# Kernel tuning notes

Hardware: AMD Instinct MI355X
Metric: run time of the kernel (lower is better)

The kernel has to match this reference:

```python
import jax, jax.numpy as jnp
import numpy as np

N_NODES = 100000
NEG_SLOPE = 0.2


def _gat_conv(x, edge_index, W, att_src, att_dst, bias):
    """Single-head PyG-style GATConv with self-loops.
    x: [N, F_in], edge_index: [2, E] (row 0 = src j, row 1 = dst i).
    """
    N = x.shape[0]
    h = x @ W  # [N, F_out]
    # add self-loops
    loop = jnp.arange(N, dtype=edge_index.dtype)
    src = jnp.concatenate([edge_index[0], loop])
    dst = jnp.concatenate([edge_index[1], loop])
    # per-node attention terms, gathered per edge
    a_s = h @ att_src  # [N]
    a_d = h @ att_dst  # [N]
    e = jax.nn.leaky_relu(a_s[src] + a_d[dst], NEG_SLOPE)  # [E+N]
    # segment softmax over incoming edges of each destination
    m = jax.ops.segment_max(e, dst, num_segments=N)  # [N]
    m = jnp.where(jnp.isfinite(m), m, 0.0)
    p = jnp.exp(e - m[dst])
    denom = jax.ops.segment_sum(p, dst, num_segments=N)  # [N], >0 due to self-loops
    alpha = p / denom[dst]  # [E+N]
    # scatter-aggregate weighted source features
    out = jax.ops.segment_sum(h[src] * alpha[:, None], dst, num_segments=N)
    return out + bias


def setup_inputs() -> dict:
    key = jax.random.key(0)
    ks = jax.random.split(key, 12)
    F_in, H, C = 128, 64, 40
    x = jax.random.normal(ks[0], (N_NODES, F_in), dtype=jnp.float32)
    edge_index = jax.random.randint(ks[1], (2, 1600000), 0, N_NODES, dtype=jnp.int64)
    s1 = 1.0 / np.sqrt(F_in)
    s2 = 1.0 / np.sqrt(H)
    return {
        "x": x,
        "edge_index": edge_index,
        "W1": jax.random.uniform(ks[2], (F_in, H), jnp.float32, -s1, s1),
        "att_src1": jax.random.uniform(ks[3], (H,), jnp.float32, -s2, s2),
        "att_dst1": jax.random.uniform(ks[4], (H,), jnp.float32, -s2, s2),
        "b1": jnp.zeros((H,), jnp.float32),
        "W2": jax.random.uniform(ks[5], (H, C), jnp.float32, -s2, s2),
        "att_src2": jax.random.uniform(ks[6], (C,), jnp.float32, -1.0 / np.sqrt(C), 1.0 / np.sqrt(C)),
        "att_dst2": jax.random.uniform(ks[7], (C,), jnp.float32, -1.0 / np.sqrt(C), 1.0 / np.sqrt(C)),
        "b2": jnp.zeros((C,), jnp.float32),
    }


def reference(x, edge_index, W1, att_src1, att_dst1, b1, W2, att_src2, att_dst2, b2):
    h = _gat_conv(x, edge_index, W1, att_src1, att_dst1, b1)
    h = jax.nn.relu(h)
    # dropout is identity in eval mode
    out = _gat_conv(h, edge_index, W2, att_src2, att_dst2, b2)
    return out
```

## Files before the change

kernel.cpp:

```cpp
#include <hip/hip_runtime.h>
#include <math.h>


#define NEG_SLOPE 0.2f
#define BIN_SHIFT 8
#define BIN_NODES 256
#define MAXBINS   512
#define CAPB      4864
#define K1_CHUNK  4096
#define MAXDEG    128
#define AGG_STRIDE 132
#define XS1 136

typedef _Float16 h4_t __attribute__((ext_vector_type(4)));
typedef _Float16 h8_t __attribute__((ext_vector_type(8)));
typedef float    f16x_t __attribute__((ext_vector_type(16)));

__device__ __forceinline__ float lrelu(float v) {
    return v > 0.f ? v : NEG_SLOPE * v;
}

__global__ __launch_bounds__(256) void prep_kernel(
    const float* __restrict__ W1, const float* __restrict__ W2,
    const float* __restrict__ as1, const float* __restrict__ ad1,
    const float* __restrict__ as2, const float* __restrict__ ad2,
    _Float16* __restrict__ w1t, _Float16* __restrict__ w2t,
    float* __restrict__ u1, float* __restrict__ v1,
    int* __restrict__ bin_cursor)
{
    const int tid = threadIdx.x;
    if (blockIdx.x == 0) {
        for (int j = tid; j < MAXBINS; j += 256) bin_cursor[j] = 0;
        for (int i = tid; i < 8192; i += 256) {
            int n = i >> 7, k = i & 127;
            w1t[i] = (_Float16)W1[k * 64 + n];
        }
        if (tid < 128) {
            float su = 0.f, sv = 0.f;
            for (int n = 0; n < 64; ++n) {
                float w = W1[tid * 64 + n];
                su += w * as1[n];
                sv += w * ad1[n];
            }
            u1[tid] = su; v1[tid] = sv;
        }
    } else {
        __shared__ float u2l[64], v2l[64];
        if (tid < 64) {
            float su = 0.f, sv = 0.f;
            for (int n = 0; n < 40; ++n) {
                float w = W2[tid * 40 + n];
                su += w * as2[n];
                sv += w * ad2[n];
            }
            u2l[tid] = su; v2l[tid] = sv;
        }
        __syncthreads();
        for (int i = tid; i < 4096; i += 256) {
            int n = i >> 6, k = i & 63;
            _Float16 o = (_Float16)0.f;
            if (n < 40)       o = (_Float16)W2[k * 40 + n];
            else if (n == 40) o = (_Float16)u2l[k];
            else if (n == 41) o = (_Float16)v2l[k];
            w2t[i] = o;
        }
    }
}

__global__ __launch_bounds__(256) void gemm1_bin_kernel(
    const float* __restrict__ x, const _Float16* __restrict__ w1t,
    const float* __restrict__ u1, const float* __restrict__ v1,
    _Float16* __restrict__ h, float* __restrict__ as_, float* __restrict__ ad_,
    int N, int gb,
    const int* __restrict__ src, const int* __restrict__ dst, int E, int nbins,
    int* __restrict__ bin_cursor, int* __restrict__ binned)
{
    __shared__ __align__(16) char smem[35840];
    const int tid = threadIdx.x;

    if (blockIdx.x < gb) {
        _Float16* Xs = (_Float16*)smem;
        _Float16* Wt = (_Float16*)(smem + 17408);
        float*    Us = (float*)(smem + 34816);
        float*    Vs = (float*)(smem + 35328);
        const int lane = tid & 63;
        const int w = tid >> 6;
        const int rh = w >> 1, ch = w & 1;
        const long rowbase = (long)blockIdx.x * 64;

        {
            const int4* s4 = (const int4*)w1t;
#pragma unroll
            for (int i = 0; i < 4; ++i) {
                int f = tid + i * 256;
                int n = f >> 4, c = f & 15;
                *(int4*)&Wt[n * XS1 + c * 8] = s4[f];
            }
        }
        {
            const float4* X4 = (const float4*)x;
            const long gmax = (long)N * 32;
#pragma unroll
            for (int i = 0; i < 8; ++i) {
                int f = tid + i * 256;
                int row = f >> 5, c4 = f & 31;
                long gi = (rowbase + row) * 32 + c4;
                float4 v = (gi < gmax) ? X4[gi] : make_float4(0.f, 0.f, 0.f, 0.f);
                h4_t hv;
                hv.x = (_Float16)v.x; hv.y = (_Float16)v.y;
                hv.z = (_Float16)v.z; hv.w = (_Float16)v.w;
                *(h4_t*)&Xs[row * XS1 + c4 * 4] = hv;
            }
        }
        if (tid < 128) Us[tid] = u1[tid];
        else { int t = tid - 128; Vs[t] = v1[t]; }
        __syncthreads();

        {
            const int arow = tid >> 2, apart = tid & 3;
            const _Float16* xr = &Xs[arow * XS1 + apart * 32];
            float ps = 0.f, pd = 0.f;
#pragma unroll
            for (int k = 0; k < 32; k += 4) {
                h4_t xv = *(const h4_t*)(xr + k);
                float4 uu = *(const float4*)&Us[apart * 32 + k];
                float4 vv = *(const float4*)&Vs[apart * 32 + k];
                float x0 = (float)xv.x, x1 = (float)xv.y, x2 = (float)xv.z, x3 = (float)xv.w;
                ps += x0 * uu.x + x1 * uu.y + x2 * uu.z + x3 * uu.w;
                pd += x0 * vv.x + x1 * vv.y + x2 * vv.z + x3 * vv.w;
            }
            ps += __shfl_xor(ps, 1); ps += __shfl_xor(ps, 2);
            pd += __shfl_xor(pd, 1); pd += __shfl_xor(pd, 2);
            if (apart == 0 && rowbase + arow < N) {
                as_[rowbase + arow] = ps;
                ad_[rowbase + arow] = pd;
            }
        }

        const int m = lane & 31, khalf = lane >> 5;
        const _Float16* ax = &Xs[(rh * 32 + m) * XS1 + khalf * 8];
        const _Float16* bx = &Wt[(ch * 32 + m) * XS1 + khalf * 8];

        f16x_t acc = {};
#pragma unroll
        for (int kc = 0; kc < 8; ++kc) {
            h8_t a = *(const h8_t*)(ax + kc * 16);
            h8_t b = *(const h8_t*)(bx + kc * 16);
            acc = __builtin_amdgcn_mfma_f32_32x32x16_f16(a, b, acc, 0, 0, 0);
        }

        const int col = ch * 32 + m;
#pragma unroll
        for (int r = 0; r < 16; ++r) {
            int rowl = (r & 3) + 8 * (r >> 2) + 4 * khalf;
            long grow = rowbase + rh * 32 + rowl;
            if (grow < N) h[grow * 64 + col] = (_Float16)acc[r];
        }
    } else {
        int* hist = (int*)smem;
        int* base = (int*)(smem + 2048);
        int* lcur = (int*)(smem + 4096);
        const int e0 = (blockIdx.x - gb) * K1_CHUNK;

        int sreg[16], dreg[16];
#pragma unroll
        for (int k = 0; k < 16; ++k) {
            int e = e0 + tid + k * 256;
            bool ok = e < E;
            dreg[k] = ok ? dst[e] : -1;
            sreg[k] = ok ? src[e] : 0;
        }

        for (int j = tid; j < nbins; j += 256) hist[j] = 0;
        __syncthreads();
#pragma unroll
        for (int k = 0; k < 16; ++k)
            if (dreg[k] >= 0) atomicAdd(&hist[dreg[k] >> BIN_SHIFT], 1);
        __syncthreads();
        for (int j = tid; j < nbins; j += 256) {
            int c = hist[j];
            base[j] = (c > 0) ? atomicAdd(&bin_cursor[j], c) : 0;
            lcur[j] = 0;
        }
        __syncthreads();
#pragma unroll
        for (int k = 0; k < 16; ++k) {
            if (dreg[k] >= 0) {
                int b = dreg[k] >> BIN_SHIFT;
                int o = atomicAdd(&lcur[b], 1);
                int pos = base[b] + o;
                if (pos < CAPB)
                    binned[b * CAPB + pos] =
                        (sreg[k] << BIN_SHIFT) | (dreg[k] & (BIN_NODES - 1));
            }
        }
    }
}

__global__ __launch_bounds__(512) void fine_kernel(
    const int* __restrict__ bin_cursor, const int* __restrict__ binned,
    int* __restrict__ csr, int* __restrict__ rowptr, int N, int nbins)
{
    __shared__ int a[MAXBINS];
    __shared__ int nh[BIN_NODES];
    __shared__ int cur[BIN_NODES];
    __shared__ int sb[2];
    const int b = blockIdx.x;
    const int tid = threadIdx.x;

    int v = (tid < nbins) ? min(bin_cursor[tid], CAPB) : 0;
    a[tid] = v;
    __syncthreads();
#pragma unroll
    for (int ofs = 1; ofs < MAXBINS; ofs <<= 1) {
        int t = (tid >= ofs) ? a[tid - ofs] : 0;
        __syncthreads();
        a[tid] += t;
        __syncthreads();
    }
    if (tid == 0) {
        sb[0] = (b > 0) ? a[b - 1] : 0;
        sb[1] = a[nbins - 1];
    }

    const int cnt = min(bin_cursor[b], CAPB);
    const int nn = min(BIN_NODES, N - b * BIN_NODES);
    const int* __restrict__ brec = binned + (long)b * CAPB;

    if (tid < BIN_NODES) nh[tid] = 0;
    __syncthreads();

    for (int k = tid; k < cnt; k += 512) {
        atomicAdd(&nh[brec[k] & (BIN_NODES - 1)], 1);
    }
    __syncthreads();

    int hv = (tid < BIN_NODES) ? nh[tid] : 0;
#pragma unroll
    for (int ofs = 1; ofs < BIN_NODES; ofs <<= 1) {
        int t = (tid >= ofs && tid < BIN_NODES) ? nh[tid - ofs] : 0;
        __syncthreads();
        if (tid < BIN_NODES) nh[tid] += t;
        __syncthreads();
    }
    const int binbase = sb[0];
    if (tid < BIN_NODES) {
        int excl = nh[tid] - hv;
        if (tid < nn) rowptr[b * BIN_NODES + tid] = binbase + excl;
        cur[tid] = binbase + excl;
    }
    if (b == nbins - 1 && tid == 0) rowptr[N] = sb[1];
    __syncthreads();

    for (int k = tid; k < cnt; k += 512) {
        int rec = brec[k];
        int pos = atomicAdd(&cur[rec & (BIN_NODES - 1)], 1);
        csr[pos] = rec >> BIN_SHIFT;
    }
}

#define XS2 72
__global__ __launch_bounds__(256) void gemm2_kernel(
    const _Float16* __restrict__ hin, const _Float16* __restrict__ w2t,
    _Float16* __restrict__ h2, float* __restrict__ as_, float* __restrict__ ad_,
    int N)
{
    __shared__ __align__(16) _Float16 Xs[64 * XS2];
    __shared__ __align__(16) _Float16 Wt[64 * XS2];
    const int tid = threadIdx.x;
    const int lane = tid & 63;
    const int w = tid >> 6;
    const int rh = w >> 1, ch = w & 1;
    const long rowbase = (long)blockIdx.x * 64;

    {
        const int4* s4 = (const int4*)w2t;
#pragma unroll
        for (int i = 0; i < 2; ++i) {
            int f = tid + i * 256;
            int n = f >> 3, c = f & 7;
            *(int4*)&Wt[n * XS2 + c * 8] = s4[f];
        }
    }
    {
        const h8_t* X8 = (const h8_t*)hin;
        const long gmax = (long)N * 8;
#pragma unroll
        for (int i = 0; i < 2; ++i) {
            int f = tid + i * 256;
            int row = f >> 3, c = f & 7;
            long gi = (rowbase + row) * 8 + c;
            h8_t v = {};
            if (gi < gmax) v = X8[gi];
#pragma unroll
            for (int j = 0; j < 8; ++j) v[j] = (v[j] > (_Float16)0.f) ? v[j] : (_Float16)0.f;
            *(h8_t*)&Xs[row * XS2 + c * 8] = v;
        }
    }
    __syncthreads();

    const int m = lane & 31, khalf = lane >> 5;
    const _Float16* ax = &Xs[(rh * 32 + m) * XS2 + khalf * 8];
    const _Float16* bx = &Wt[(ch * 32 + m) * XS2 + khalf * 8];

    f16x_t acc = {};
#pragma unroll
    for (int kc = 0; kc < 4; ++kc) {
        h8_t a = *(const h8_t*)(ax + kc * 16);
        h8_t b = *(const h8_t*)(bx + kc * 16);
        acc = __builtin_amdgcn_mfma_f32_32x32x16_f16(a, b, acc, 0, 0, 0);
    }

    const int col = ch * 32 + m;
#pragma unroll
    for (int r = 0; r < 16; ++r) {
        int rowl = (r & 3) + 8 * (r >> 2) + 4 * khalf;
        long grow = rowbase + rh * 32 + rowl;
        float v = acc[r];
        if (grow < N) {
            if (col < 40)       h2[grow * 40 + col] = (_Float16)v;
            else if (col == 40) as_[grow] = v;
            else if (col == 41) ad_[grow] = v;
        }
    }
}

template<int F, typename OT>
__global__ __launch_bounds__(256) void aggregate_kernel(
    const _Float16* __restrict__ h, const float* __restrict__ as_,
    const float* __restrict__ ad_, const int* __restrict__ rowptr,
    const int* __restrict__ csr, const float* __restrict__ bias,
    OT* __restrict__ out, int N)
{
    __shared__ int   Ss[16 * AGG_STRIDE];
    __shared__ float Ps[16 * AGG_STRIDE];
    const int tid = threadIdx.x;
    const int dl  = tid >> 4;
    const int sub = tid & 15;
    const int i = blockIdx.x * 16 + dl;
    const bool alive = (i < N);

    int r0 = 0, deg = 0;
    if (alive) {
        r0 = rowptr[i];
        deg = rowptr[i + 1] - r0;
        if (deg > MAXDEG) deg = MAXDEG;
    }
    const float adi    = alive ? ad_[i] : 0.f;
    const float e_self = alive ? lrelu(as_[i] + adi) : 0.f;

    int*   __restrict__ sp = &Ss[dl * AGG_STRIDE];
    float* __restrict__ pp = &Ps[dl * AGG_STRIDE];

    float psum = 0.f;
    for (int c = sub; c < deg; c += 16) {
        int s = csr[r0 + c];
        float p = __expf(lrelu(as_[s] + adi));
        sp[c] = s;
        pp[c] = p;
        psum += p;
    }
#pragma unroll
    for (int off = 1; off < 16; off <<= 1) psum += __shfl_xor(psum, off);
    const float p_self = __expf(e_self);
    const float inv = 1.f / (psum + p_self);

    const bool act = (sub * 4 < F);
    const int  col = act ? sub * 4 : 0;
    float4 acc = make_float4(0.f, 0.f, 0.f, 0.f);

    int k = 0;
    for (; k + 4 <= deg; k += 4) {
        int   sA = sp[k],     sB = sp[k + 1], sC = sp[k + 2], sD = sp[k + 3];
        float pA = pp[k],     pB = pp[k + 1], pC = pp[k + 2], pD = pp[k + 3];
        if (act) {
            h4_t hA = *(const h4_t*)&h[(long)sA * F + col];
            h4_t hB = *(const h4_t*)&h[(long)sB * F + col];
            h4_t hC = *(const h4_t*)&h[(long)sC * F + col];
            h4_t hD = *(const h4_t*)&h[(long)sD * F + col];
            acc.x += (float)hA.x * pA + (float)hB.x * pB + (float)hC.x * pC + (float)hD.x * pD;
            acc.y += (float)hA.y * pA + (float)hB.y * pB + (float)hC.y * pC + (float)hD.y * pD;
            acc.z += (float)hA.z * pA + (float)hB.z * pB + (float)hC.z * pC + (float)hD.z * pD;
            acc.w += (float)hA.w * pA + (float)hB.w * pB + (float)hC.w * pC + (float)hD.w * pD;
        }
    }
    for (; k < deg; ++k) {
        int   s = sp[k];
        float p = pp[k];
        if (act) {
            h4_t hv = *(const h4_t*)&h[(long)s * F + col];
            acc.x += (float)hv.x * p; acc.y += (float)hv.y * p;
            acc.z += (float)hv.z * p; acc.w += (float)hv.w * p;
        }
    }

    if (alive && act) {
        h4_t hv = *(const h4_t*)&h[(long)i * F + col];
        float4 bv = *(const float4*)&bias[col];
        float ox = (acc.x + (float)hv.x * p_self) * inv + bv.x;
        float oy = (acc.y + (float)hv.y * p_self) * inv + bv.y;
        float oz = (acc.z + (float)hv.z * p_self) * inv + bv.z;
        float ow = (acc.w + (float)hv.w * p_self) * inv + bv.w;
        if constexpr (sizeof(OT) == 4) {
            float4 o = make_float4(ox, oy, oz, ow);
            *(float4*)&out[(long)i * F + col] = o;
        } else {
            h4_t o;
            o.x = (_Float16)ox; o.y = (_Float16)oy;
            o.z = (_Float16)oz; o.w = (_Float16)ow;
            *(h4_t*)&out[(long)i * F + col] = o;
        }
    }
}

extern "C" void kernel_launch(void* const* d_in, const int* in_sizes, int n_in,
                              void* d_out, int out_size, void* d_ws, size_t ws_size,
                              hipStream_t stream) {
    const float* x    = (const float*)d_in[0];
    const int*   ei   = (const int*)d_in[1];
    const float* W1   = (const float*)d_in[2];
    const float* at_s1= (const float*)d_in[3];
    const float* at_d1= (const float*)d_in[4];
    const float* b1   = (const float*)d_in[5];
    const float* W2   = (const float*)d_in[6];
    const float* at_s2= (const float*)d_in[7];
    const float* at_d2= (const float*)d_in[8];
    const float* b2   = (const float*)d_in[9];
    float* out = (float*)d_out;

    const int N = in_sizes[0] / 128;
    const int E = in_sizes[1] / 2;
    const int nbins = (N + BIN_NODES - 1) >> BIN_SHIFT;

    char* p = (char*)d_ws;
    auto carve = [&](size_t bytes) -> void* {
        void* r = (void*)p;
        p += (bytes + 255) & ~(size_t)255;
        return r;
    };
    int*       bin_cursor = (int*)      carve((size_t)MAXBINS * 4);
    int*       binned     = (int*)      carve((size_t)nbins * CAPB * 4);
    int*       csr        = (int*)      carve((size_t)E * 4);
    int*       rowptr     = (int*)      carve((size_t)(N + 1) * 4);
    _Float16*  w1t        = (_Float16*) carve((size_t)8192 * 2);
    _Float16*  w2t        = (_Float16*) carve((size_t)4096 * 2);
    float*     u1         = (float*)    carve((size_t)128 * 4);
    float*     v1         = (float*)    carve((size_t)128 * 4);
    _Float16*  h1         = (_Float16*) carve((size_t)N * 64 * 2);
    _Float16*  agg1h      = (_Float16*) carve((size_t)N * 64 * 2);
    _Float16*  h2         = (_Float16*) carve((size_t)N * 40 * 2);
    float*     asn        = (float*)    carve((size_t)N * 4);
    float*     adn        = (float*)    carve((size_t)N * 4);

    prep_kernel<<<2, 256, 0, stream>>>(W1, W2, at_s1, at_d1, at_s2, at_d2,
                                       w1t, w2t, u1, v1, bin_cursor);

    const int gb = (N + 63) / 64;
    const int bb = (E + K1_CHUNK - 1) / K1_CHUNK;
    gemm1_bin_kernel<<<gb + bb, 256, 0, stream>>>(
        x, w1t, u1, v1, h1, asn, adn, N, gb,
        ei, ei + E, E, nbins, bin_cursor, binned);

    fine_kernel<<<nbins, 512, 0, stream>>>(bin_cursor, binned, csr, rowptr, N, nbins);

    aggregate_kernel<64, _Float16><<<(N + 15) / 16, 256, 0, stream>>>(
        h1, asn, adn, rowptr, csr, b1, agg1h, N);

    gemm2_kernel<<<(N + 63) / 64, 256, 0, stream>>>(agg1h, w2t, h2, asn, adn, N);

    aggregate_kernel<40, float><<<(N + 15) / 16, 256, 0, stream>>>(
        h2, asn, adn, rowptr, csr, b2, out, N);
}
```

Measured before the change: 233.3 us.

## Fuse layer-1 aggregation with layer-2 GEMM and reorder binning blocks first

Merges the layer-1 neighbour aggregation and the second GEMM into one kernel. Each 16-lane group aggregates one node, then multiplies the ReLU'd row by W2 through shuffles and shared-memory weights, so the intermediate agg1 buffer is never written to or read back from global memory and one launch is removed. It also reorders the combined gemm1/binning grid so the edge-binning blocks are scheduled before the GEMM blocks. The GEMM moves from MFMA to scalar FMAs per node, and layer-2 attention scalars go to separate buffers.

```diff
diff --git a/kernel.cpp b/kernel.cpp
--- a/kernel.cpp
+++ b/kernel.cpp
@@ -71,14 +71,14 @@
     const float* __restrict__ x, const _Float16* __restrict__ w1t,
     const float* __restrict__ u1, const float* __restrict__ v1,
     _Float16* __restrict__ h, float* __restrict__ as_, float* __restrict__ ad_,
-    int N, int gb,
+    int N, int bb,
     const int* __restrict__ src, const int* __restrict__ dst, int E, int nbins,
     int* __restrict__ bin_cursor, int* __restrict__ binned)
 {
     __shared__ __align__(16) char smem[35840];
     const int tid = threadIdx.x;
 
-    if (blockIdx.x < gb) {
+    if ((int)blockIdx.x >= bb) {
         _Float16* Xs = (_Float16*)smem;
         _Float16* Wt = (_Float16*)(smem + 17408);
         float*    Us = (float*)(smem + 34816);
@@ -86,7 +86,7 @@
         const int lane = tid & 63;
         const int w = tid >> 6;
         const int rh = w >> 1, ch = w & 1;
-        const long rowbase = (long)blockIdx.x * 64;
+        const long rowbase = (long)(blockIdx.x - bb) * 64;
 
         {
             const int4* s4 = (const int4*)w1t;
@@ -160,7 +160,7 @@
         int* hist = (int*)smem;
         int* base = (int*)(smem + 2048);
         int* lcur = (int*)(smem + 4096);
-        const int e0 = (blockIdx.x - gb) * K1_CHUNK;
+        const int e0 = blockIdx.x * K1_CHUNK;
 
         int sreg[16], dreg[16];
 #pragma unroll
@@ -259,69 +259,110 @@
     }
 }
 
-#define XS2 72
-__global__ __launch_bounds__(256) void gemm2_kernel(
-    const _Float16* __restrict__ hin, const _Float16* __restrict__ w2t,
-    _Float16* __restrict__ h2, float* __restrict__ as_, float* __restrict__ ad_,
+__global__ __launch_bounds__(256) void agg1_gemm2_kernel(
+    const _Float16* __restrict__ h, const float* __restrict__ as_,
+    const float* __restrict__ ad_, const int* __restrict__ rowptr,
+    const int* __restrict__ csr, const float* __restrict__ b1,
+    const _Float16* __restrict__ w2t,
+    _Float16* __restrict__ h2, float* __restrict__ as2, float* __restrict__ ad2,
     int N)
 {
-    __shared__ __align__(16) _Float16 Xs[64 * XS2];
-    __shared__ __align__(16) _Float16 Wt[64 * XS2];
+    __shared__ int   Ss[16 * AGG_STRIDE];
+    __shared__ float Ps[16 * AGG_STRIDE];
+    __shared__ h4_t  W2s[48 * 16];
     const int tid = threadIdx.x;
-    const int lane = tid & 63;
-    const int w = tid >> 6;
-    const int rh = w >> 1, ch = w & 1;
-    const long rowbase = (long)blockIdx.x * 64;
-
-    {
-        const int4* s4 = (const int4*)w2t;
-#pragma unroll
-        for (int i = 0; i < 2; ++i) {
-            int f = tid + i * 256;
-            int n = f >> 3, c = f & 7;
-            *(int4*)&Wt[n * XS2 + c * 8] = s4[f];
-        }
-    }
-    {
-        const h8_t* X8 = (const h8_t*)hin;
-        const long gmax = (long)N * 8;
-#pragma unroll
-        for (int i = 0; i < 2; ++i) {
-            int f = tid + i * 256;
-            int row = f >> 3, c = f & 7;
-            long gi = (rowbase + row) * 8 + c;
-            h8_t v = {};
-            if (gi < gmax) v = X8[gi];
-#pragma unroll
-            for (int j = 0; j < 8; ++j) v[j] = (v[j] > (_Float16)0.f) ? v[j] : (_Float16)0.f;
-            *(h8_t*)&Xs[row * XS2 + c * 8] = v;
-        }
+    const int dl  = tid >> 4;
+    const int sub = tid & 15;
+    const int i = blockIdx.x * 16 + dl;
+    const bool alive = (i < N);
+
+    for (int idx = tid; idx < 768; idx += 256) {
+        int n = idx >> 4, q = idx & 15;
+        W2s[idx] = *(const h4_t*)&w2t[n * 64 + q * 4];
     }
     __syncthreads();
 
-    const int m = lane & 31, khalf = lane >> 5;
-    const _Float16* ax = &Xs[(rh * 32 + m) * XS2 + khalf * 8];
-    const _Float16* bx = &Wt[(ch * 32 + m) * XS2 + khalf * 8];
-
-    f16x_t acc = {};
-#pragma unroll
-    for (int kc = 0; kc < 4; ++kc) {
-        h8_t a = *(const h8_t*)(ax + kc * 16);
-        h8_t b = *(const h8_t*)(bx + kc * 16);
-        acc = __builtin_amdgcn_mfma_f32_32x32x16_f16(a, b, acc, 0, 0, 0);
-    }
-
-    const int col = ch * 32 + m;
-#pragma unroll
-    for (int r = 0; r < 16; ++r) {
-        int rowl = (r & 3) + 8 * (r >> 2) + 4 * khalf;
-        long grow = rowbase + rh * 32 + rowl;
-        float v = acc[r];
-        if (grow < N) {
-            if (col < 40)       h2[grow * 40 + col] = (_Float16)v;
-            else if (col == 40) as_[grow] = v;
-            else if (col == 41) ad_[grow] = v;
-        }
+    int r0 = 0, deg = 0;
+    if (alive) {
+        r0 = rowptr[i];
+        deg = rowptr[i + 1] - r0;
+        if (deg > MAXDEG) deg = MAXDEG;
+    }
+    const float adi    = alive ? ad_[i] : 0.f;
+    const float e_self = alive ? lrelu(as_[i] + adi) : 0.f;
+
+    int*   __restrict__ sp = &Ss[dl * AGG_STRIDE];
+    float* __restrict__ pp = &Ps[dl * AGG_STRIDE];
+
+    float psum = 0.f;
+    for (int c = sub; c < deg; c += 16) {
+        int s = csr[r0 + c];
+        float p = __expf(lrelu(as_[s] + adi));
+        sp[c] = s;
+        pp[c] = p;
+        psum += p;
+    }
+#pragma unroll
+    for (int off = 1; off < 16; off <<= 1) psum += __shfl_xor(psum, off);
+    const float p_self = __expf(e_self);
+    const float inv = 1.f / (psum + p_self);
+
+    const int col = sub * 4;
+    float4 acc = make_float4(0.f, 0.f, 0.f, 0.f);
+
+    int k = 0;
+    for (; k + 4 <= deg; k += 4) {
+        int   sA = sp[k],     sB = sp[k + 1], sC = sp[k + 2], sD = sp[k + 3];
+        float pA = pp[k],     pB = pp[k + 1], pC = pp[k + 2], pD = pp[k + 3];
+        h4_t hA = *(const h4_t*)&h[(long)sA * 64 + col];
+        h4_t hB = *(const h4_t*)&h[(long)sB * 64 + col];
+        h4_t hC = *(const h4_t*)&h[(long)sC * 64 + col];
+        h4_t hD = *(const h4_t*)&h[(long)sD * 64 + col];
+        acc.x += (float)hA.x * pA + (float)hB.x * pB + (float)hC.x * pC + (float)hD.x * pD;
+        acc.y += (float)hA.y * pA + (float)hB.y * pB + (float)hC.y * pC + (float)hD.y * pD;
+        acc.z += (float)hA.z * pA + (float)hB.z * pB + (float)hC.z * pC + (float)hD.z * pD;
+        acc.w += (float)hA.w * pA + (float)hB.w * pB + (float)hC.w * pC + (float)hD.w * pD;
+    }
+    for (; k < deg; ++k) {
+        int   s = sp[k];
+        float p = pp[k];
+        h4_t hv = *(const h4_t*)&h[(long)s * 64 + col];
+        acc.x += (float)hv.x * p; acc.y += (float)hv.y * p;
+        acc.z += (float)hv.z * p; acc.w += (float)hv.w * p;
+    }
+
+    h4_t hv = {};
+    if (alive) hv = *(const h4_t*)&h[(long)i * 64 + col];
+    float4 bv = *(const float4*)&b1[col];
+    const float rx = fmaxf((acc.x + (float)hv.x * p_self) * inv + bv.x, 0.f);
+    const float ry = fmaxf((acc.y + (float)hv.y * p_self) * inv + bv.y, 0.f);
+    const float rz = fmaxf((acc.z + (float)hv.z * p_self) * inv + bv.z, 0.f);
+    const float rw = fmaxf((acc.w + (float)hv.w * p_self) * inv + bv.w, 0.f);
+
+    const int n0 = sub, n1 = sub + 16, n2 = sub + 32;
+    float y0 = 0.f, y1 = 0.f, y2 = 0.f;
+#pragma unroll
+    for (int t = 0; t < 16; ++t) {
+        const int s = (sub + t) & 15;
+        const float vx = __shfl(rx, s, 16);
+        const float vy = __shfl(ry, s, 16);
+        const float vz = __shfl(rz, s, 16);
+        const float vw = __shfl(rw, s, 16);
+        h4_t w0 = W2s[n0 * 16 + s];
+        h4_t w1 = W2s[n1 * 16 + s];
+        h4_t w2 = W2s[n2 * 16 + s];
+        y0 += vx * (float)w0.x + vy * (float)w0.y + vz * (float)w0.z + vw * (float)w0.w;
+        y1 += vx * (float)w1.x + vy * (float)w1.y + vz * (float)w1.z + vw * (float)w1.w;
+        y2 += vx * (float)w2.x + vy * (float)w2.y + vz * (float)w2.z + vw * (float)w2.w;
+    }
+
+    if (alive) {
+        const long ob = (long)i * 40;
+        h2[ob + n0] = (_Float16)y0;
+        h2[ob + n1] = (_Float16)y1;
+        if (sub < 8)       h2[ob + n2] = (_Float16)y2;
+        else if (sub == 8) as2[i] = y2;
+        else if (sub == 9) ad2[i] = y2;
     }
 }
 
@@ -447,10 +488,11 @@
     float*     u1         = (float*)    carve((size_t)128 * 4);
     float*     v1         = (float*)    carve((size_t)128 * 4);
     _Float16*  h1         = (_Float16*) carve((size_t)N * 64 * 2);
-    _Float16*  agg1h      = (_Float16*) carve((size_t)N * 64 * 2);
     _Float16*  h2         = (_Float16*) carve((size_t)N * 40 * 2);
     float*     asn        = (float*)    carve((size_t)N * 4);
     float*     adn        = (float*)    carve((size_t)N * 4);
+    float*     as2n       = (float*)    carve((size_t)N * 4);
+    float*     ad2n       = (float*)    carve((size_t)N * 4);
 
     prep_kernel<<<2, 256, 0, stream>>>(W1, W2, at_s1, at_d1, at_s2, at_d2,
                                        w1t, w2t, u1, v1, bin_cursor);
@@ -458,16 +500,14 @@
     const int gb = (N + 63) / 64;
     const int bb = (E + K1_CHUNK - 1) / K1_CHUNK;
     gemm1_bin_kernel<<<gb + bb, 256, 0, stream>>>(
-        x, w1t, u1, v1, h1, asn, adn, N, gb,
+        x, w1t, u1, v1, h1, asn, adn, N, bb,
         ei, ei + E, E, nbins, bin_cursor, binned);
 
     fine_kernel<<<nbins, 512, 0, stream>>>(bin_cursor, binned, csr, rowptr, N, nbins);
 
-    aggregate_kernel<64, _Float16><<<(N + 15) / 16, 256, 0, stream>>>(
-        h1, asn, adn, rowptr, csr, b1, agg1h, N);
-
-    gemm2_kernel<<<(N + 63) / 64, 256, 0, stream>>>(agg1h, w2t, h2, asn, adn, N);
+    agg1_gemm2_kernel<<<(N + 15) / 16, 256, 0, stream>>>(
+        h1, asn, adn, rowptr, csr, b1, w2t, h2, as2n, ad2n, N);
 
     aggregate_kernel<40, float><<<(N + 15) / 16, 256, 0, stream>>>(
-        h2, asn, adn, rowptr, csr, b2, out, N);
-}
+        h2, as2n, ad2n, rowptr, csr, b2, out, N);
+}
```

After: 252.6 us. +8.3%, slower.
